# Performance work log

Hardware: AMD Instinct MI355X
Metric: run time of the kernel (lower is better)

Reference implementation:

```python
import jax, jax.numpy as jnp
import numpy as np

N, E = 50000, 800000
IN_C, HID_C, OUT_C, HEADS = 128, 32, 16, 4
NEG_SLOPE = 0.2


def gat_conv(x, src, dst, W, att_src, att_dst, bias, heads, out_ch, concat, n_nodes):
    # linear transform: [N, heads, out_ch]
    h = (x @ W).reshape(n_nodes, heads, out_ch)
    # per-node attention logits [N, heads]
    a_s = (h * att_src).sum(-1)
    a_d = (h * att_dst).sum(-1)
    # per-edge raw attention (edge j->i uses src logit of j, dst logit of i)
    alpha = jax.nn.leaky_relu(a_s[src] + a_d[dst], negative_slope=NEG_SLOPE)  # [E, heads]
    # segment softmax over destination neighborhoods
    amax = jax.ops.segment_max(alpha, dst, num_segments=n_nodes)
    ex = jnp.exp(alpha - amax[dst])
    den = jax.ops.segment_sum(ex, dst, num_segments=n_nodes)
    coef = ex / den[dst]  # [E, heads]
    # weighted scatter-add aggregation
    msg = h[src] * coef[:, :, None]  # [E, heads, out_ch]
    out = jax.ops.segment_sum(msg, dst, num_segments=n_nodes)  # [N, heads, out_ch]
    out = out.reshape(n_nodes, heads * out_ch) if concat else out.mean(axis=1)
    return out + bias


def setup_inputs() -> dict:
    key = jax.random.key(0)
    ks = jax.random.split(key, 10)
    x = jax.random.normal(ks[0], (N, IN_C), dtype=jnp.float32)
    edge_index = jax.random.randint(ks[1], (2, E), 0, N, dtype=jnp.int64)
    s1 = 1.0 / np.sqrt(IN_C)
    s2 = 1.0 / np.sqrt(HID_C * HEADS)
    W1 = jax.random.normal(ks[2], (IN_C, HEADS * HID_C), dtype=jnp.float32) * s1
    att_src1 = jax.random.normal(ks[3], (HEADS, HID_C), dtype=jnp.float32) * s1
    att_dst1 = jax.random.normal(ks[4], (HEADS, HID_C), dtype=jnp.float32) * s1
    b1 = jnp.zeros((HEADS * HID_C,), dtype=jnp.float32)
    W2 = jax.random.normal(ks[5], (HEADS * HID_C, OUT_C), dtype=jnp.float32) * s2
    att_src2 = jax.random.normal(ks[6], (1, OUT_C), dtype=jnp.float32) * s2
    att_dst2 = jax.random.normal(ks[7], (1, OUT_C), dtype=jnp.float32) * s2
    b2 = jnp.zeros((OUT_C,), dtype=jnp.float32)
    return {"x": x, "edge_index": edge_index, "W1": W1, "att_src1": att_src1,
            "att_dst1": att_dst1, "b1": b1, "W2": W2, "att_src2": att_src2,
            "att_dst2": att_dst2, "b2": b2}


def reference(x, edge_index, W1, att_src1, att_dst1, b1, W2, att_src2, att_dst2, b2):
    n = x.shape[0]
    # PyG GATConv default: add self loops
    ar = jnp.arange(n, dtype=edge_index.dtype)
    src = jnp.concatenate([edge_index[0], ar])
    dst = jnp.concatenate([edge_index[1], ar])
    h = gat_conv(x, src, dst, W1, att_src1, att_dst1, b1, HEADS, HID_C, True, n)
    h = jax.nn.elu(h)
    out = gat_conv(h, src, dst, W2, att_src2, att_dst2, b2, 1, OUT_C, False, n)
    return out
```

## Files before the change

kernel.cpp:

```cpp
#include <hip/hip_runtime.h>

typedef __attribute__((ext_vector_type(8))) short short8;
typedef __attribute__((ext_vector_type(4))) float f32x4;
typedef __attribute__((ext_vector_type(2))) float f32x2;

#define CAP 64

__device__ __forceinline__ float lrelu02(float a) { return a > 0.0f ? a : 0.2f * a; }

__device__ __forceinline__ unsigned bf16rne(float f) {
    unsigned u = __float_as_uint(f);
    return (u + 0x7fffu + ((u >> 16) & 1u)) >> 16;
}

__global__ __launch_bounds__(256) void k_build(
    const int* __restrict__ ei, int* __restrict__ deg, int* __restrict__ col, int E)
{
    int tid = blockIdx.x * blockDim.x + threadIdx.x;
    int nthr = gridDim.x * blockDim.x;
    int E4 = E & ~3;
    for (int b = tid * 4; b < E4; b += nthr * 4) {
        int4 d = *(const int4*)(ei + E + b);
        int4 s = *(const int4*)(ei + b);
        int r0 = atomicAdd(&deg[d.x], 1);
        int r1 = atomicAdd(&deg[d.y], 1);
        int r2 = atomicAdd(&deg[d.z], 1);
        int r3 = atomicAdd(&deg[d.w], 1);
        if (r0 < CAP) col[d.x * CAP + r0] = s.x;
        if (r1 < CAP) col[d.y * CAP + r1] = s.y;
        if (r2 < CAP) col[d.z * CAP + r2] = s.z;
        if (r3 < CAP) col[d.w * CAP + r3] = s.w;
    }
    for (int e = E4 + tid; e < E; e += nthr) {
        int d = ei[E + e];
        int r = atomicAdd(&deg[d], 1);
        if (r < CAP) col[d * CAP + r] = ei[e];
    }
}

__global__ __launch_bounds__(256) void k_gemm1(
    const float* __restrict__ x, const float* __restrict__ W,
    const float* __restrict__ attS, const float* __restrict__ attD,
    unsigned short* __restrict__ h1, float* __restrict__ as1, float* __restrict__ ad1,
    int4* __restrict__ degz, int n4, int N)
{
    __shared__ unsigned short Wt[128 * 128];
    __shared__ unsigned short xs[64 * 128];

    const int t = threadIdx.x;
    const int lane = t & 63;
    const int wv = t >> 6;
    const int ln = lane & 15;
    const int lg = lane >> 4;
    const int r0 = blockIdx.x * 64;

    for (int i = blockIdx.x * 256 + t; i < n4; i += gridDim.x * 256)
        degz[i] = make_int4(0, 0, 0, 0);

    #pragma unroll
    for (int i = 0; i < 16; ++i) {
        int flat = i * 256 + t;
        int n = flat & 127;
        int k0 = (flat >> 7) * 4;
        float v0 = W[(size_t)(k0 + 0) * 128 + n];
        float v1 = W[(size_t)(k0 + 1) * 128 + n];
        float v2 = W[(size_t)(k0 + 2) * 128 + n];
        float v3 = W[(size_t)(k0 + 3) * 128 + n];
        uint2 pk;
        pk.x = bf16rne(v0) | (bf16rne(v1) << 16);
        pk.y = bf16rne(v2) | (bf16rne(v3) << 16);
        int byteo = n * 256 + ((k0 * 2) ^ ((n & 7) << 4));
        *(uint2*)((char*)Wt + byteo) = pk;
    }
    {
        int mbase = t >> 5, k0 = (t & 31) * 4;
        #pragma unroll
        for (int it = 0; it < 8; ++it) {
            int m = mbase + it * 8;
            int rr = r0 + m;
            float4 v = make_float4(0.f, 0.f, 0.f, 0.f);
            if (rr < N) v = *(const float4*)&x[(size_t)rr * 128 + k0];
            unsigned lo = bf16rne(v.x) | (bf16rne(v.y) << 16);
            unsigned hi = bf16rne(v.z) | (bf16rne(v.w) << 16);
            int byteo = m * 256 + ((k0 * 2) ^ ((m & 7) << 4));
            *(uint2*)((char*)xs + byteo) = make_uint2(lo, hi);
        }
    }
    __syncthreads();

    f32x4 acc[8];
    #pragma unroll
    for (int i = 0; i < 8; ++i) acc[i] = (f32x4)(0.f);

    #pragma unroll
    for (int kk = 0; kk < 4; ++kk) {
        int kb = (kk * 32 + lg * 8) * 2;
        int am = wv * 16 + ln;
        short8 a = *(const short8*)((char*)xs + am * 256 + (kb ^ ((am & 7) << 4)));
        #pragma unroll
        for (int tile = 0; tile < 8; ++tile) {
            int n = tile * 16 + ln;
            short8 b = *(const short8*)((char*)Wt + n * 256 + (kb ^ ((n & 7) << 4)));
            acc[tile] = __builtin_amdgcn_mfma_f32_16x16x32_bf16(a, b, acc[tile], 0, 0, 0);
        }
    }

    float aSt[8], aDt[8];
    #pragma unroll
    for (int tile = 0; tile < 8; ++tile) {
        aSt[tile] = attS[tile * 16 + ln];
        aDt[tile] = attD[tile * 16 + ln];
    }
    #pragma unroll
    for (int r = 0; r < 4; ++r) {
        int row = r0 + wv * 16 + lg * 4 + r;
        #pragma unroll
        for (int h = 0; h < 4; ++h) {
            float s = acc[2*h][r] * aSt[2*h] + acc[2*h+1][r] * aSt[2*h+1];
            float d = acc[2*h][r] * aDt[2*h] + acc[2*h+1][r] * aDt[2*h+1];
            s += __shfl_xor(s, 1); s += __shfl_xor(s, 2); s += __shfl_xor(s, 4); s += __shfl_xor(s, 8);
            d += __shfl_xor(d, 1); d += __shfl_xor(d, 2); d += __shfl_xor(d, 4); d += __shfl_xor(d, 8);
            if (ln == h * 4 + r && row < N) {
                as1[row * 4 + h] = s;
                ad1[row * 4 + h] = d;
            }
        }
    }

    __syncthreads();
    #pragma unroll
    for (int tile = 0; tile < 8; ++tile) {
        #pragma unroll
        for (int r = 0; r < 4; ++r) {
            int m = wv * 16 + lg * 4 + r;
            int byteo = m * 256 + (((tile * 16 + ln) * 2) ^ ((m & 7) << 4));
            *(unsigned short*)((char*)xs + byteo) = (unsigned short)bf16rne(acc[tile][r]);
        }
    }
    __syncthreads();
    #pragma unroll
    for (int it = 0; it < 4; ++it) {
        int idx = t + it * 256;
        int m = idx >> 4, o = idx & 15;
        int byteo = m * 256 + ((o * 16) ^ ((m & 7) << 4));
        if (r0 + m < N)
            *(uint4*)((char*)(h1 + (size_t)(r0 + m) * 128) + o * 16) =
                *(const uint4*)((const char*)xs + byteo);
    }
}

__global__ __launch_bounds__(256) void k_agg1(
    const unsigned short* __restrict__ h1, const float* __restrict__ as1,
    const float* __restrict__ ad1, const int* __restrict__ degv,
    const int* __restrict__ col, const float* __restrict__ b1,
    const int* __restrict__ ei, int E,
    unsigned short* __restrict__ out1, int N)
{
    int wid = (int)(((unsigned)blockIdx.x * blockDim.x + threadIdx.x) >> 6);
    if (wid >= N) return;
    int lane = threadIdx.x & 63;
    int deg = degv[wid];
    int start = wid * CAP;
    const float4 ad = *(const float4*)(ad1 + (size_t)wid * 4);
    int head = lane >> 4;
    float adh = head == 0 ? ad.x : head == 1 ? ad.y : head == 2 ? ad.z : ad.w;

    float aself = as1[(size_t)wid * 4 + head];
    float vself = __expf(lrelu02(aself + adh));
    unsigned hvs = *(const unsigned*)(h1 + (size_t)wid * 128 + lane * 2);

    f32x2 acc2 = (f32x2)(0.f);

    if (deg <= CAP) {
        int idx = lane & 15;
        float ex[4];
        int sv[4];
        float den = 0.f;
        #pragma unroll
        for (int b = 0; b < 4; ++b) {
            int j = b * 16 + idx;
            float v = 0.f;
            int sc = 0;
            if (j < deg) {
                sc = col[start + j];
                v = __expf(lrelu02(as1[(size_t)sc * 4 + head] + adh));
            }
            sv[b] = sc;
            ex[b] = v;
            den += v;
        }
        den += __shfl_xor(den, 1); den += __shfl_xor(den, 2);
        den += __shfl_xor(den, 4); den += __shfl_xor(den, 8);
        den += vself;
        float rden = 1.f / den;
        #pragma unroll
        for (int b = 0; b < 4; ++b) ex[b] *= rden;
        {
            float cs = vself * rden;
            f32x2 hs;
            hs.x = __uint_as_float(hvs << 16);
            hs.y = __uint_as_float(hvs & 0xffff0000u);
            acc2 += (f32x2)(cs) * hs;
        }
        int srcbase = lane & 48;

        #pragma unroll
        for (int b = 0; b < 4; ++b) {
            int rem = deg - b * 16;
            if (rem <= 0) break;
            if (rem >= 16) {
                int sq[16]; float cf[16]; unsigned hv[16];
                #pragma unroll
                for (int q = 0; q < 16; ++q) {
                    sq[q] = __builtin_amdgcn_readlane(sv[b], q);
                    cf[q] = __shfl(ex[b], srcbase | q);
                }
                #pragma unroll
                for (int q = 0; q < 16; ++q)
                    hv[q] = *(const unsigned*)(h1 + (size_t)sq[q] * 128 + lane * 2);
                #pragma unroll
                for (int q = 0; q < 16; ++q) {
                    f32x2 h2v;
                    h2v.x = __uint_as_float(hv[q] << 16);
                    h2v.y = __uint_as_float(hv[q] & 0xffff0000u);
                    acc2 += (f32x2)(cf[q]) * h2v;
                }
            } else {
                #pragma unroll
                for (int c4 = 0; c4 < 4; ++c4) {
                    if (c4 * 4 >= rem) break;
                    int sq[4]; float cf[4]; unsigned hv[4];
                    #pragma unroll
                    for (int jj = 0; jj < 4; ++jj) {
                        int q = c4 * 4 + jj;
                        sq[jj] = __builtin_amdgcn_readlane(sv[b], q);
                        cf[jj] = __shfl(ex[b], srcbase | q);
                    }
                    #pragma unroll
                    for (int jj = 0; jj < 4; ++jj)
                        hv[jj] = *(const unsigned*)(h1 + (size_t)sq[jj] * 128 + lane * 2);
                    #pragma unroll
                    for (int jj = 0; jj < 4; ++jj) {
                        f32x2 h2v;
                        h2v.x = __uint_as_float(hv[jj] << 16);
                        h2v.y = __uint_as_float(hv[jj] & 0xffff0000u);
                        acc2 += (f32x2)(cf[jj]) * h2v;
                    }
                }
            }
        }
    } else {
        float den = vself;
        for (int e = lane; e < E; e += 64) {
            if (ei[E + e] == wid)
                den += __expf(lrelu02(as1[(size_t)ei[e] * 4 + head] + adh));
        }
        #pragma unroll
        for (int m = 8; m >= 1; m >>= 1) den += __shfl_xor(den, m);
        float rden = 1.f / den;
        {
            float cs = vself * rden;
            f32x2 hs;
            hs.x = __uint_as_float(hvs << 16);
            hs.y = __uint_as_float(hvs & 0xffff0000u);
            acc2 += (f32x2)(cs) * hs;
        }
        for (int e = 0; e < E; ++e) {
            int d = ei[E + e];
            if (d != wid) continue;
            int src = ei[e];
            float coef = __expf(lrelu02(as1[(size_t)src * 4 + head] + adh)) * rden;
            unsigned hv = *(const unsigned*)(h1 + (size_t)src * 128 + lane * 2);
            f32x2 h2v;
            h2v.x = __uint_as_float(hv << 16);
            h2v.y = __uint_as_float(hv & 0xffff0000u);
            acc2 += (f32x2)(coef) * h2v;
        }
    }

    int c0 = lane * 2;
    float o0 = acc2.x + b1[c0];
    float o1 = acc2.y + b1[c0 + 1];
    o0 = o0 > 0.f ? o0 : expm1f(o0);
    o1 = o1 > 0.f ? o1 : expm1f(o1);
    unsigned ov = bf16rne(o0) | (bf16rne(o1) << 16);
    *(unsigned*)((char*)out1 + (size_t)wid * 256 + lane * 4) = ov;
}

__global__ __launch_bounds__(256) void k_gemm2(
    const unsigned short* __restrict__ in, const float* __restrict__ W,
    const float* __restrict__ attS, const float* __restrict__ attD,
    float* __restrict__ h2, float* __restrict__ as2, float* __restrict__ ad2, int N)
{
    __shared__ unsigned short Wt[16 * 128];
    __shared__ unsigned short xs[64 * 128];
    const int t = threadIdx.x;
    const int lane = t & 63;
    const int wv = t >> 6;
    const int ln = lane & 15;
    const int lg = lane >> 4;
    const int r0 = blockIdx.x * 64;

    #pragma unroll
    for (int i = 0; i < 2; ++i) {
        int flat = i * 256 + t;
        int n = flat & 15;
        int k0 = (flat >> 4) * 4;
        float v0 = W[(size_t)(k0 + 0) * 16 + n];
        float v1 = W[(size_t)(k0 + 1) * 16 + n];
        float v2 = W[(size_t)(k0 + 2) * 16 + n];
        float v3 = W[(size_t)(k0 + 3) * 16 + n];
        uint2 pk;
        pk.x = bf16rne(v0) | (bf16rne(v1) << 16);
        pk.y = bf16rne(v2) | (bf16rne(v3) << 16);
        int byteo = n * 256 + ((k0 * 2) ^ ((n & 7) << 4));
        *(uint2*)((char*)Wt + byteo) = pk;
    }
    #pragma unroll
    for (int it = 0; it < 4; ++it) {
        int idx = t + it * 256;
        int m = idx >> 4, o = idx & 15;
        int rr = r0 + m;
        uint4 v = make_uint4(0, 0, 0, 0);
        if (rr < N) v = *(const uint4*)((const char*)(in + (size_t)rr * 128) + o * 16);
        int byteo = m * 256 + ((o * 16) ^ ((m & 7) << 4));
        *(uint4*)((char*)xs + byteo) = v;
    }
    __syncthreads();

    f32x4 acc = (f32x4)(0.f);
    #pragma unroll
    for (int kk = 0; kk < 4; ++kk) {
        int kb = (kk * 32 + lg * 8) * 2;
        int am = wv * 16 + ln;
        short8 a = *(const short8*)((char*)xs + am * 256 + (kb ^ ((am & 7) << 4)));
        short8 b = *(const short8*)((char*)Wt + ln * 256 + (kb ^ ((ln & 7) << 4)));
        acc = __builtin_amdgcn_mfma_f32_16x16x32_bf16(a, b, acc, 0, 0, 0);
    }

    float aSv = attS[ln], aDv = attD[ln];
    #pragma unroll
    for (int r = 0; r < 4; ++r) {
        int row = r0 + wv * 16 + lg * 4 + r;
        float s = acc[r] * aSv;
        float d = acc[r] * aDv;
        s += __shfl_xor(s, 1); s += __shfl_xor(s, 2); s += __shfl_xor(s, 4); s += __shfl_xor(s, 8);
        d += __shfl_xor(d, 1); d += __shfl_xor(d, 2); d += __shfl_xor(d, 4); d += __shfl_xor(d, 8);
        if (row < N) {
            h2[(size_t)row * 16 + ln] = acc[r];
            if (ln == 0) { as2[row] = s; ad2[row] = d; }
        }
    }
}

__global__ __launch_bounds__(256) void k_agg2(
    const float* __restrict__ h2, const float* __restrict__ as2,
    const float* __restrict__ ad2, const int* __restrict__ degv,
    const int* __restrict__ col, const float* __restrict__ b2,
    const int* __restrict__ ei, int E,
    float* __restrict__ out, int N)
{
    int wid = (int)(((unsigned)blockIdx.x * blockDim.x + threadIdx.x) >> 6);
    if (wid >= N) return;
    int lane = threadIdx.x & 63;
    int deg = degv[wid];
    int start = wid * CAP;
    float adv = ad2[wid];
    int sub = lane >> 4, c = lane & 15;
    float vself = __expf(lrelu02(as2[wid] + adv));
    float acc = 0.f;

    if (deg <= CAP) {
        float ex0 = 0.f;
        if (lane < deg) ex0 = __expf(lrelu02(as2[col[start + lane]] + adv));
        float den = ex0;
        #pragma unroll
        for (int m = 32; m >= 1; m >>= 1) den += __shfl_xor(den, m);
        den += vself;
        float rden = 1.f / den;
        ex0 *= rden;
        if (sub == 0) acc = fmaf(vself * rden, h2[(size_t)wid * 16 + c], acc);
        #pragma unroll
        for (int g = 0; g < 4; ++g) {
            if (g * 16 >= deg) break;
            int s[4]; float cf[4], hv[4];
            #pragma unroll
            for (int jj = 0; jj < 4; ++jj) {
                int j = g * 16 + jj * 4 + sub;
                s[jj]  = col[start + (j < deg ? j : 0)];
                cf[jj] = __shfl(ex0, j);
            }
            #pragma unroll
            for (int jj = 0; jj < 4; ++jj)
                hv[jj] = h2[(size_t)s[jj] * 16 + c];
            #pragma unroll
            for (int jj = 0; jj < 4; ++jj)
                acc = fmaf(cf[jj], hv[jj], acc);
        }
    } else {
        float den = vself;
        for (int e = lane; e < E; e += 64)
            if (ei[E + e] == wid) den += __expf(lrelu02(as2[ei[e]] + adv));
        #pragma unroll
        for (int m = 32; m >= 1; m >>= 1) den += __shfl_xor(den, m);
        float rden = 1.f / den;
        if (sub == 0) acc = fmaf(vself * rden, h2[(size_t)wid * 16 + c], acc);
        for (int e = 0; e < E; ++e) {
            int d = ei[E + e];
            if (d != wid) continue;
            int src = ei[e];
            float coef = __expf(lrelu02(as2[src] + adv)) * rden;
            if (sub == 0) acc = fmaf(coef, h2[(size_t)src * 16 + c], acc);
        }
    }

    acc += __shfl_xor(acc, 16);
    acc += __shfl_xor(acc, 32);
    if (lane < 16) out[(size_t)wid * 16 + lane] = acc + b2[lane];
}

extern "C" void kernel_launch(void* const* d_in, const int* in_sizes, int n_in,
                              void* d_out, int out_size, void* d_ws, size_t ws_size,
                              hipStream_t stream)
{
    const float* x   = (const float*)d_in[0];
    const int*   ei  = (const int*)d_in[1];
    const float* W1  = (const float*)d_in[2];
    const float* aS1 = (const float*)d_in[3];
    const float* aD1 = (const float*)d_in[4];
    const float* b1  = (const float*)d_in[5];
    const float* W2  = (const float*)d_in[6];
    const float* aS2 = (const float*)d_in[7];
    const float* aD2 = (const float*)d_in[8];
    const float* b2  = (const float*)d_in[9];
    float* out = (float*)d_out;

    int N = in_sizes[0] / 128;
    int E = in_sizes[1] / 2;
    int G1 = (N + 63) / 64;

    char* w = (char*)d_ws;
    auto alloc = [&](size_t bytes) -> void* {
        void* p = (void*)w;
        w += (bytes + 255) & ~(size_t)255;
        return p;
    };
    unsigned short* h1   = (unsigned short*)alloc((size_t)N * 128 * 2);
    unsigned short* out1 = (unsigned short*)alloc((size_t)N * 128 * 2);
    float* as1   = (float*)alloc((size_t)N * 4 * 4);
    float* ad1   = (float*)alloc((size_t)N * 4 * 4);
    float* h2    = (float*)alloc((size_t)N * 16 * 4);
    float* as2v  = (float*)alloc((size_t)N * 4);
    float* ad2v  = (float*)alloc((size_t)N * 4);
    int* deg     = (int*)alloc((size_t)(N + 4) * 4);
    int* col     = (int*)alloc((size_t)N * CAP * 4);

    const int tb = 256;
    int n4 = (N + 3) / 4;

    k_gemm1<<<G1, tb, 0, stream>>>(x, W1, aS1, aD1, h1, as1, ad1,
                                   (int4*)deg, n4, N);
    k_build<<<2048, tb, 0, stream>>>(ei, deg, col, E);
    k_agg1 <<<(N + 3) / 4, tb, 0, stream>>>(h1, as1, ad1, deg, col, b1, ei, E, out1, N);
    k_gemm2<<<G1, tb, 0, stream>>>(out1, W2, aS2, aD2, h2, as2v, ad2v, N);
    k_agg2 <<<(N + 3) / 4, tb, 0, stream>>>(h2, as2v, ad2v, deg, col, b2, ei, E, out, N);
}
```

Measured before the change: 138.5 us.

## Shard the CSR build's degree counters across eight copies to cut atomic contention

The adjacency build now uses eight separate degree-counter arrays, picked by block index, each owning a 16-slot region of a 128-slot row per node. This spreads atomic traffic on the same degree counter across eight copies. Both aggregation kernels rebuild the total degree by prefix-summing the eight shard counts and map each logical neighbor index to its shard slot. agg2 also reuses the loaded column index through a shuffle instead of reloading it. The costs are a larger, sparser column array, more index arithmetic per neighbor, and a fallback full-edge scan whenever any single shard overflows 16 entries.

```diff
diff --git a/kernel.cpp b/kernel.cpp
--- a/kernel.cpp
+++ b/kernel.cpp
@@ -4,7 +4,8 @@
 typedef __attribute__((ext_vector_type(4))) float f32x4;
 typedef __attribute__((ext_vector_type(2))) float f32x2;
 
-#define CAP 64
+#define CAPS 16
+#define CAPT 128
 
 __device__ __forceinline__ float lrelu02(float a) { return a > 0.0f ? a : 0.2f * a; }
 
@@ -14,27 +15,30 @@
 }
 
 __global__ __launch_bounds__(256) void k_build(
-    const int* __restrict__ ei, int* __restrict__ deg, int* __restrict__ col, int E)
+    const int* __restrict__ ei, int* __restrict__ deg8, int* __restrict__ col, int E, int N)
 {
+    const int shard = blockIdx.x & 7;
+    int* __restrict__ dc = deg8 + (size_t)shard * N;
+    const int sbase = shard * CAPS;
     int tid = blockIdx.x * blockDim.x + threadIdx.x;
     int nthr = gridDim.x * blockDim.x;
     int E4 = E & ~3;
     for (int b = tid * 4; b < E4; b += nthr * 4) {
         int4 d = *(const int4*)(ei + E + b);
         int4 s = *(const int4*)(ei + b);
-        int r0 = atomicAdd(&deg[d.x], 1);
-        int r1 = atomicAdd(&deg[d.y], 1);
-        int r2 = atomicAdd(&deg[d.z], 1);
-        int r3 = atomicAdd(&deg[d.w], 1);
-        if (r0 < CAP) col[d.x * CAP + r0] = s.x;
-        if (r1 < CAP) col[d.y * CAP + r1] = s.y;
-        if (r2 < CAP) col[d.z * CAP + r2] = s.z;
-        if (r3 < CAP) col[d.w * CAP + r3] = s.w;
+        int r0 = atomicAdd(&dc[d.x], 1);
+        int r1 = atomicAdd(&dc[d.y], 1);
+        int r2 = atomicAdd(&dc[d.z], 1);
+        int r3 = atomicAdd(&dc[d.w], 1);
+        if (r0 < CAPS) col[d.x * CAPT + sbase + r0] = s.x;
+        if (r1 < CAPS) col[d.y * CAPT + sbase + r1] = s.y;
+        if (r2 < CAPS) col[d.z * CAPT + sbase + r2] = s.z;
+        if (r3 < CAPS) col[d.w * CAPT + sbase + r3] = s.w;
     }
     for (int e = E4 + tid; e < E; e += nthr) {
         int d = ei[E + e];
-        int r = atomicAdd(&deg[d], 1);
-        if (r < CAP) col[d * CAP + r] = ei[e];
+        int r = atomicAdd(&dc[d], 1);
+        if (r < CAPS) col[d * CAPT + sbase + r] = ei[e];
     }
 }
 
@@ -151,7 +155,7 @@
 
 __global__ __launch_bounds__(256) void k_agg1(
     const unsigned short* __restrict__ h1, const float* __restrict__ as1,
-    const float* __restrict__ ad1, const int* __restrict__ degv,
+    const float* __restrict__ ad1, const int* __restrict__ deg8,
     const int* __restrict__ col, const float* __restrict__ b1,
     const int* __restrict__ ei, int E,
     unsigned short* __restrict__ out1, int N)
@@ -159,19 +163,32 @@
     int wid = (int)(((unsigned)blockIdx.x * blockDim.x + threadIdx.x) >> 6);
     if (wid >= N) return;
     int lane = threadIdx.x & 63;
-    int deg = degv[wid];
-    int start = wid * CAP;
     const float4 ad = *(const float4*)(ad1 + (size_t)wid * 4);
     int head = lane >> 4;
     float adh = head == 0 ? ad.x : head == 1 ? ad.y : head == 2 ? ad.z : ad.w;
 
+    int cl = 0;
+    if (lane < 8) cl = deg8[(size_t)lane * N + wid];
+    int cnt[8], p[8];
+    int pf = 0;
+    bool fits = true;
+    #pragma unroll
+    for (int c = 0; c < 8; ++c) {
+        int v = __shfl(cl, c);
+        cnt[c] = v;
+        p[c] = pf;
+        pf += v;
+        fits = fits && (v <= CAPS);
+    }
+    int deg = pf;
+
     float aself = as1[(size_t)wid * 4 + head];
     float vself = __expf(lrelu02(aself + adh));
     unsigned hvs = *(const unsigned*)(h1 + (size_t)wid * 128 + lane * 2);
 
     f32x2 acc2 = (f32x2)(0.f);
 
-    if (deg <= CAP) {
+    if (deg <= 64 && fits) {
         int idx = lane & 15;
         float ex[4];
         int sv[4];
@@ -182,7 +199,13 @@
             float v = 0.f;
             int sc = 0;
             if (j < deg) {
-                sc = col[start + j];
+                int off = 0;
+                #pragma unroll
+                for (int c = 0; c < 8; ++c) {
+                    bool in = (j >= p[c]) && (j < p[c] + cnt[c]);
+                    if (in) off = c * CAPS + (j - p[c]);
+                }
+                sc = col[wid * CAPT + off];
                 v = __expf(lrelu02(as1[(size_t)sc * 4 + head] + adh));
             }
             sv[b] = sc;
@@ -251,12 +274,12 @@
         }
     } else {
         float den = vself;
-        for (int e = lane; e < E; e += 64) {
+        for (int e = (lane & 15); e < E; e += 16) {
             if (ei[E + e] == wid)
                 den += __expf(lrelu02(as1[(size_t)ei[e] * 4 + head] + adh));
         }
-        #pragma unroll
-        for (int m = 8; m >= 1; m >>= 1) den += __shfl_xor(den, m);
+        den += __shfl_xor(den, 1); den += __shfl_xor(den, 2);
+        den += __shfl_xor(den, 4); den += __shfl_xor(den, 8);
         float rden = 1.f / den;
         {
             float cs = vself * rden;
@@ -355,7 +378,7 @@
 
 __global__ __launch_bounds__(256) void k_agg2(
     const float* __restrict__ h2, const float* __restrict__ as2,
-    const float* __restrict__ ad2, const int* __restrict__ degv,
+    const float* __restrict__ ad2, const int* __restrict__ deg8,
     const int* __restrict__ col, const float* __restrict__ b2,
     const int* __restrict__ ei, int E,
     float* __restrict__ out, int N)
@@ -363,16 +386,39 @@
     int wid = (int)(((unsigned)blockIdx.x * blockDim.x + threadIdx.x) >> 6);
     if (wid >= N) return;
     int lane = threadIdx.x & 63;
-    int deg = degv[wid];
-    int start = wid * CAP;
     float adv = ad2[wid];
     int sub = lane >> 4, c = lane & 15;
     float vself = __expf(lrelu02(as2[wid] + adv));
     float acc = 0.f;
 
-    if (deg <= CAP) {
+    int cl = 0;
+    if (lane < 8) cl = deg8[(size_t)lane * N + wid];
+    int cnt[8], p[8];
+    int pf = 0;
+    bool fits = true;
+    #pragma unroll
+    for (int cc2 = 0; cc2 < 8; ++cc2) {
+        int v = __shfl(cl, cc2);
+        cnt[cc2] = v;
+        p[cc2] = pf;
+        pf += v;
+        fits = fits && (v <= CAPS);
+    }
+    int deg = pf;
+
+    if (deg <= 64 && fits) {
         float ex0 = 0.f;
-        if (lane < deg) ex0 = __expf(lrelu02(as2[col[start + lane]] + adv));
+        int cv = 0;
+        if (lane < deg) {
+            int off = 0;
+            #pragma unroll
+            for (int cc2 = 0; cc2 < 8; ++cc2) {
+                bool in = (lane >= p[cc2]) && (lane < p[cc2] + cnt[cc2]);
+                if (in) off = cc2 * CAPS + (lane - p[cc2]);
+            }
+            cv = col[wid * CAPT + off];
+            ex0 = __expf(lrelu02(as2[cv] + adv));
+        }
         float den = ex0;
         #pragma unroll
         for (int m = 32; m >= 1; m >>= 1) den += __shfl_xor(den, m);
@@ -387,7 +433,7 @@
             #pragma unroll
             for (int jj = 0; jj < 4; ++jj) {
                 int j = g * 16 + jj * 4 + sub;
-                s[jj]  = col[start + (j < deg ? j : 0)];
+                s[jj]  = __shfl(cv, j);
                 cf[jj] = __shfl(ex0, j);
             }
             #pragma unroll
@@ -452,16 +498,16 @@
     float* h2    = (float*)alloc((size_t)N * 16 * 4);
     float* as2v  = (float*)alloc((size_t)N * 4);
     float* ad2v  = (float*)alloc((size_t)N * 4);
-    int* deg     = (int*)alloc((size_t)(N + 4) * 4);
-    int* col     = (int*)alloc((size_t)N * CAP * 4);
+    int* deg8    = (int*)alloc((size_t)N * 8 * 4);
+    int* col     = (int*)alloc((size_t)N * CAPT * 4);
 
     const int tb = 256;
-    int n4 = (N + 3) / 4;
+    int n4 = (N * 8 + 3) / 4;
 
     k_gemm1<<<G1, tb, 0, stream>>>(x, W1, aS1, aD1, h1, as1, ad1,
-                                   (int4*)deg, n4, N);
-    k_build<<<2048, tb, 0, stream>>>(ei, deg, col, E);
-    k_agg1 <<<(N + 3) / 4, tb, 0, stream>>>(h1, as1, ad1, deg, col, b1, ei, E, out1, N);
+                                   (int4*)deg8, n4, N);
+    k_build<<<2048, tb, 0, stream>>>(ei, deg8, col, E, N);
+    k_agg1 <<<(N + 3) / 4, tb, 0, stream>>>(h1, as1, ad1, deg8, col, b1, ei, E, out1, N);
     k_gemm2<<<G1, tb, 0, stream>>>(out1, W2, aS2, aD2, h2, as2v, ad2v, N);
-    k_agg2 <<<(N + 3) / 4, tb, 0, stream>>>(h2, as2v, ad2v, deg, col, b2, ei, E, out, N);
-}
+    k_agg2 <<<(N + 3) / 4, tb, 0, stream>>>(h2, as2v, ad2v, deg8, col, b2, ei, E, out, N);
+}
```

Measured after the change: 149.8 us. 1.08x slower.
